# Kernel tuning notes

Hardware: AMD Instinct MI355X
Metric: run time of the kernel (lower is better)

The kernel has to match this reference:

```python
import jax, jax.numpy as jnp
import numpy as np

ALPHA = 0.2  # LeakyReLU negative slope
NEG_INF = -1e12


def setup_inputs() -> dict:
    key = jax.random.key(0)
    k1, k2, k3, k4, k5 = jax.random.split(key, 5)
    N, F = 4096, 512
    inp = jax.random.normal(k1, (N, F), dtype=jnp.float32)
    adj = jax.random.randint(k2, (N, N), 0, 2).astype(jnp.float32)
    W = jax.random.normal(k3, (F, F), dtype=jnp.float32) * (1.414 / np.sqrt(F))
    a = jax.random.normal(k4, (2 * F, 1), dtype=jnp.float32) * 0.05
    wtrans = jax.random.normal(k5, (2 * F, F), dtype=jnp.float32) * (1.414 / np.sqrt(1.5 * F))
    return {"inp": inp, "adj": adj, "W": W, "a": a, "wtrans": wtrans}


def reference(inp, adj, W, a, wtrans):
    F_out = W.shape[1]
    h = inp @ W                                   # [N, F]
    Wh1 = h @ a[:F_out, :]                        # [N, 1]
    Wh2 = h @ a[F_out:, :]                        # [N, 1]
    e = jax.nn.leaky_relu(Wh1 + Wh2.T, ALPHA)     # [N, N]
    mask = adj > 0
    attention = jax.nn.softmax(jnp.where(mask, e, NEG_INF), axis=1)
    negative_attention = -jax.nn.softmax(jnp.where(mask, -e, NEG_INF), axis=1)
    # dropout p=0.0 (eval mode): identity
    h_prime = attention @ inp                     # [N, F_in]
    h_prime_negative = negative_attention @ inp   # [N, F_in]
    h_prime_double = jnp.concatenate([h_prime, h_prime_negative], axis=1)
    new_h_prime = h_prime_double @ wtrans         # [N, F_out]
    return jax.nn.elu(new_h_prime)
```

## Files before the change

kernel.cpp:

```cpp
#include <hip/hip_runtime.h>
#include <hip/hip_bf16.h>

#define N_NODES 4096
#define F_DIM   512
#define KTOT    8192
#define KSPLIT  8
#define LOG2E   1.44269504f

typedef __attribute__((ext_vector_type(8))) short bf16x8;
typedef __attribute__((ext_vector_type(4))) float f32x4;

__device__ inline unsigned short f2bf(float f) {
  union { float f; unsigned u; } c; c.f = f;
  unsigned r = c.u + 0x7fffu + ((c.u >> 16) & 1u);
  return (unsigned short)(r >> 16);
}
__device__ inline float bf2f(unsigned short u) {
  union { unsigned u; float f; } c; c.u = ((unsigned)u) << 16;
  return c.f;
}

__global__ void k_compute_v(const float* __restrict__ W, const float* __restrict__ a,
                            float* __restrict__ v1, float* __restrict__ v2) {
  int r = blockIdx.x, l = threadIdx.x;
  float s1 = 0.f, s2 = 0.f;
  for (int c = l; c < F_DIM; c += 64) {
    float w = W[(size_t)r * F_DIM + c];
    s1 += w * a[c];
    s2 += w * a[F_DIM + c];
  }
#pragma unroll
  for (int off = 32; off > 0; off >>= 1) { s1 += __shfl_down(s1, off); s2 += __shfl_down(s2, off); }
  if (l == 0) { v1[r] = s1; v2[r] = s2; }
}

__global__ void k_compute_wh(const float* __restrict__ inp, const float* __restrict__ v1,
                             const float* __restrict__ v2, float* __restrict__ Wh1,
                             float* __restrict__ Wh2) {
  int i = blockIdx.x, l = threadIdx.x;
  float s1 = 0.f, s2 = 0.f;
  for (int c = l; c < F_DIM; c += 64) {
    float x = inp[(size_t)i * F_DIM + c];
    s1 += x * v1[c];
    s2 += x * v2[c];
  }
#pragma unroll
  for (int off = 32; off > 0; off >>= 1) { s1 += __shfl_down(s1, off); s2 += __shfl_down(s2, off); }
  if (l == 0) { Wh1[i] = s1 * LOG2E; Wh2[i] = s2 * LOG2E; }
}

__global__ void k_transpose_bf16(const float* __restrict__ src, unsigned short* __restrict__ dst,
                                 int R, int C) {
  __shared__ float tile[32][33];
  int c0 = blockIdx.x * 32, r0 = blockIdx.y * 32;
  int tx = threadIdx.x, ty = threadIdx.y;
#pragma unroll
  for (int i = ty; i < 32; i += 8)
    tile[i][tx] = src[(size_t)(r0 + i) * C + c0 + tx];
  __syncthreads();
#pragma unroll
  for (int i = ty; i < 32; i += 8)
    dst[(size_t)(c0 + i) * R + r0 + tx] = f2bf(tile[tx][i]);
}

__global__ __launch_bounds__(256) void k_y(const float* __restrict__ inp,
                                           const unsigned short* __restrict__ wtT,
                                           unsigned short* __restrict__ YT) {
  int tid = threadIdx.x, l = tid & 63, w = tid >> 6;
  int row = l & 15, kg = l >> 4;
  int jt = blockIdx.x * 64 + w * 16;
  int cb = blockIdx.y * 64;
  f32x4 acc1[4] = {}, acc2[4] = {};
  const float* ap = inp + (size_t)(jt + row) * F_DIM + kg * 8;
  for (int k0 = 0; k0 < F_DIM; k0 += 32) {
    float4 f0 = *(const float4*)(ap + k0);
    float4 f1 = *(const float4*)(ap + k0 + 4);
    bf16x8 a;
    a[0] = (short)f2bf(f0.x); a[1] = (short)f2bf(f0.y); a[2] = (short)f2bf(f0.z); a[3] = (short)f2bf(f0.w);
    a[4] = (short)f2bf(f1.x); a[5] = (short)f2bf(f1.y); a[6] = (short)f2bf(f1.z); a[7] = (short)f2bf(f1.w);
#pragma unroll
    for (int n = 0; n < 4; n++) {
      const unsigned short* bp = wtT + (size_t)(cb + n * 16 + row) * 1024 + kg * 8 + k0;
      bf16x8 b1 = *(const bf16x8*)(bp);
      bf16x8 b2 = *(const bf16x8*)(bp + F_DIM);
      acc1[n] = __builtin_amdgcn_mfma_f32_16x16x32_bf16(a, b1, acc1[n], 0, 0, 0);
      acc2[n] = __builtin_amdgcn_mfma_f32_16x16x32_bf16(a, b2, acc2[n], 0, 0, 0);
    }
  }
  int jb = jt + kg * 4;
#pragma unroll
  for (int n = 0; n < 4; n++) {
    int f = cb + n * 16 + row;
    ushort4 o1, o2;
    o1.x = f2bf(acc1[n][0]); o1.y = f2bf(acc1[n][1]); o1.z = f2bf(acc1[n][2]); o1.w = f2bf(acc1[n][3]);
    o2.x = f2bf(acc2[n][0]); o2.y = f2bf(acc2[n][1]); o2.z = f2bf(acc2[n][2]); o2.w = f2bf(acc2[n][3]);
    *(ushort4*)(YT + (size_t)f * KTOT + jb) = o1;
    *(ushort4*)(YT + (size_t)f * KTOT + 4096 + jb) = o2;
  }
}

__global__ __launch_bounds__(256) void k_p(const float* __restrict__ adj,
                                           const float* __restrict__ Wh1,
                                           const float* __restrict__ Wh2,
                                           unsigned short* __restrict__ Pcat) {
  int i = blockIdx.x, t = threadIdx.x;
  float w1 = Wh1[i];
  int j0 = t * 16;
  const float* ar = adj + (size_t)i * N_NODES + j0;
  float4 A0 = *(const float4*)(ar);
  float4 A1 = *(const float4*)(ar + 4);
  float4 A2 = *(const float4*)(ar + 8);
  float4 A3 = *(const float4*)(ar + 12);
  float am[16] = {A0.x, A0.y, A0.z, A0.w, A1.x, A1.y, A1.z, A1.w,
                  A2.x, A2.y, A2.z, A2.w, A3.x, A3.y, A3.z, A3.w};
  float4 wv0 = *(const float4*)(Wh2 + j0);
  float4 wv1 = *(const float4*)(Wh2 + j0 + 4);
  float4 wv2 = *(const float4*)(Wh2 + j0 + 8);
  float4 wv3 = *(const float4*)(Wh2 + j0 + 12);
  float w2[16] = {wv0.x, wv0.y, wv0.z, wv0.w, wv1.x, wv1.y, wv1.z, wv1.w,
                  wv2.x, wv2.y, wv2.z, wv2.w, wv3.x, wv3.y, wv3.z, wv3.w};
  float pe[16], ne[16];
  float sp = 0.f, sn = 0.f;
#pragma unroll
  for (int r = 0; r < 16; r++) {
    float s = w1 + w2[r];
    float e = fmaxf(s, 0.2f * s);
    float p = exp2f(e);
    float n = exp2f(-e);
    if (!(am[r] > 0.f)) { p = 0.f; n = 0.f; }
    pe[r] = p; ne[r] = n; sp += p; sn += n;
  }
#pragma unroll
  for (int off = 1; off < 64; off <<= 1) { sp += __shfl_xor(sp, off); sn += __shfl_xor(sn, off); }
  __shared__ float red[2][4];
  int wv = t >> 6, ln = t & 63;
  if (ln == 0) { red[0][wv] = sp; red[1][wv] = sn; }
  __syncthreads();
  sp = red[0][0] + red[0][1] + red[0][2] + red[0][3];
  sn = red[1][0] + red[1][1] + red[1][2] + red[1][3];
  float rp = 1.f / sp;
  float rn = -1.f / sn;
  bf16x8 o;
#pragma unroll
  for (int r = 0; r < 8; r++) o[r] = (short)f2bf(pe[r] * rp);
  *(bf16x8*)(Pcat + (size_t)i * KTOT + j0) = o;
#pragma unroll
  for (int r = 0; r < 8; r++) o[r] = (short)f2bf(pe[8 + r] * rp);
  *(bf16x8*)(Pcat + (size_t)i * KTOT + j0 + 8) = o;
#pragma unroll
  for (int r = 0; r < 8; r++) o[r] = (short)f2bf(ne[r] * rn);
  *(bf16x8*)(Pcat + (size_t)i * KTOT + 4096 + j0) = o;
#pragma unroll
  for (int r = 0; r < 8; r++) o[r] = (short)f2bf(ne[8 + r] * rn);
  *(bf16x8*)(Pcat + (size_t)i * KTOT + 4096 + j0 + 8) = o;
}

#define GLOAD16(gp, lp) __builtin_amdgcn_global_load_lds( \
    (const __attribute__((address_space(1))) unsigned int*)(gp), \
    (__attribute__((address_space(3))) unsigned int*)(lp), 16, 0, 0)

__global__ __launch_bounds__(256) void k_pv(const unsigned short* __restrict__ Pcat,
                                            const unsigned short* __restrict__ YT,
                                            unsigned short* __restrict__ part) {
  __shared__ unsigned short Ab[2][128 * 32];
  __shared__ unsigned short Bb[2][128 * 32];
  const int kchunk = KTOT / KSPLIT;
  int t = threadIdx.x;
  int l = t & 63, w = t >> 6;
  int la = l & 15, kg = l >> 4;
  int wr = w >> 1, wc = w & 1;
  int bm0 = blockIdx.x * 128, bn0 = blockIdx.y * 128;
  size_t kbase = (size_t)blockIdx.z * kchunk;
  const int nsteps = kchunk / 32;

  int seg = ((t & 3) ^ ((t >> 3) & 3)) << 4;
  const char* gA = (const char*)Pcat + ((size_t)(bm0 + (t >> 2)) * KTOT + kbase) * 2 + seg;
  const char* gB = (const char*)YT   + ((size_t)(bn0 + (t >> 2)) * KTOT + kbase) * 2 + seg;
  const size_t rstep = (size_t)64 * KTOT * 2;

  int aswz = (kg ^ ((la >> 1) & 3)) << 4;
  int abase = (wr * 64 + la) * 64 + aswz;
  int bbase = (wc * 64 + la) * 64 + aswz;

  f32x4 acc[4][4] = {};

#define STAGE(buf, st) do { \
    const char* _ga = gA + (size_t)(st) * 64; \
    const char* _gb = gB + (size_t)(st) * 64; \
    char* _la = (char*)&Ab[buf][0] + w * 1024; \
    char* _lb = (char*)&Bb[buf][0] + w * 1024; \
    GLOAD16(_ga, _la); \
    GLOAD16(_ga + rstep, _la + 4096); \
    GLOAD16(_gb, _lb); \
    GLOAD16(_gb + rstep, _lb + 4096); \
  } while (0)

  STAGE(0, 0);
  __syncthreads();
  for (int st = 0; st < nsteps; st++) {
    int cur = st & 1;
    if (st + 1 < nsteps) STAGE(cur ^ 1, st + 1);
    const char* Abp = (const char*)&Ab[cur][0];
    const char* Bbp = (const char*)&Bb[cur][0];
    bf16x8 af[4], bfr[4];
#pragma unroll
    for (int mi = 0; mi < 4; mi++) af[mi] = *(const bf16x8*)(Abp + abase + mi * 16 * 64);
#pragma unroll
    for (int ni = 0; ni < 4; ni++) bfr[ni] = *(const bf16x8*)(Bbp + bbase + ni * 16 * 64);
#pragma unroll
    for (int mi = 0; mi < 4; mi++)
#pragma unroll
      for (int ni = 0; ni < 4; ni++)
        acc[mi][ni] = __builtin_amdgcn_mfma_f32_16x16x32_bf16(af[mi], bfr[ni], acc[mi][ni], 0, 0, 0);
    __syncthreads();
  }

  unsigned short* po = part + (size_t)blockIdx.z * (N_NODES * F_DIM);
#pragma unroll
  for (int mi = 0; mi < 4; mi++)
#pragma unroll
    for (int ni = 0; ni < 4; ni++)
#pragma unroll
      for (int r = 0; r < 4; r++) {
        int i_ = bm0 + wr * 64 + mi * 16 + kg * 4 + r;
        int f_ = bn0 + wc * 64 + ni * 16 + la;
        po[(size_t)i_ * F_DIM + f_] = f2bf(acc[mi][ni][r]);
      }
}

__global__ __launch_bounds__(256) void k_fin(const unsigned short* __restrict__ part,
                                             float* __restrict__ out) {
  size_t idx = ((size_t)blockIdx.x * 256 + threadIdx.x) * 8;
  float s[8] = {};
#pragma unroll
  for (int p = 0; p < KSPLIT; p++) {
    bf16x8 v = *(const bf16x8*)(part + (size_t)p * (N_NODES * F_DIM) + idx);
#pragma unroll
    for (int r = 0; r < 8; r++) s[r] += bf2f((unsigned short)v[r]);
  }
#pragma unroll
  for (int r = 0; r < 8; r++) s[r] = s[r] > 0.f ? s[r] : (__expf(s[r]) - 1.f);
  float4 o0 = make_float4(s[0], s[1], s[2], s[3]);
  float4 o1 = make_float4(s[4], s[5], s[6], s[7]);
  *(float4*)(out + idx) = o0;
  *(float4*)(out + idx + 4) = o1;
}

extern "C" void kernel_launch(void* const* d_in, const int* in_sizes, int n_in,
                              void* d_out, int out_size, void* d_ws, size_t ws_size,
                              hipStream_t stream) {
  (void)in_sizes; (void)n_in; (void)out_size; (void)ws_size;
  const float* inp    = (const float*)d_in[0];
  const float* adj    = (const float*)d_in[1];
  const float* W      = (const float*)d_in[2];
  const float* a      = (const float*)d_in[3];
  const float* wtrans = (const float*)d_in[4];
  float* out = (float*)d_out;

  char* ws = (char*)d_ws;
  float* v1  = (float*)ws;
  float* v2  = (float*)(ws + 2048);
  float* Wh1 = (float*)(ws + 4096);
  float* Wh2 = (float*)(ws + 20480);

  const size_t PSZ = (size_t)N_NODES * F_DIM * 2;
  char* regA = ws + 65536;
  unsigned short* wtT  = (unsigned short*)regA;
  unsigned short* part = (unsigned short*)regA;
  unsigned short* YT   = (unsigned short*)(regA + KSPLIT * PSZ);
  unsigned short* Pcat = (unsigned short*)(regA + KSPLIT * PSZ + 8388608);

  k_compute_v<<<512, 64, 0, stream>>>(W, a, v1, v2);
  k_compute_wh<<<4096, 64, 0, stream>>>(inp, v1, v2, Wh1, Wh2);
  k_transpose_bf16<<<dim3(16, 32), dim3(32, 8), 0, stream>>>(wtrans, wtT, 1024, F_DIM);
  k_y<<<dim3(64, 8), 256, 0, stream>>>(inp, wtT, YT);
  k_p<<<4096, 256, 0, stream>>>(adj, Wh1, Wh2, Pcat);
  k_pv<<<dim3(32, 4, KSPLIT), 256, 0, stream>>>(Pcat, YT, part);
  k_fin<<<1024, 256, 0, stream>>>(part, out);
}
```

Measured before the change: 136.4 us.

## Enlarge PV GEMM tiles to 256x256 with triple-buffered async LDS pipeline

Doubles the split-K PV GEMM block tile to 256x256 with 512 threads (8 waves, each computing 128x64). LDS staging moves from double to triple buffering, with explicit vmcnt waits and raw barriers in place of a full syncthreads. MFMA sections are raised in priority with s_setprio. The goal is more data reuse per loaded byte and better overlap of global-to-LDS loads with MFMA work. In exchange the grid shrinks to 256 blocks, and register and LDS use per block grow.

```diff
diff --git a/kernel.cpp b/kernel.cpp
--- a/kernel.cpp
+++ b/kernel.cpp
@@ -159,70 +159,81 @@
     (const __attribute__((address_space(1))) unsigned int*)(gp), \
     (__attribute__((address_space(3))) unsigned int*)(lp), 16, 0, 0)
 
-__global__ __launch_bounds__(256) void k_pv(const unsigned short* __restrict__ Pcat,
-                                            const unsigned short* __restrict__ YT,
-                                            unsigned short* __restrict__ part) {
-  __shared__ unsigned short Ab[2][128 * 32];
-  __shared__ unsigned short Bb[2][128 * 32];
+__global__ __launch_bounds__(512, 2) void k_pv(const unsigned short* __restrict__ Pcat,
+                                               const unsigned short* __restrict__ YT,
+                                               unsigned short* __restrict__ part) {
+  __shared__ unsigned short Ab[3][256 * 32];
+  __shared__ unsigned short Bb[3][256 * 32];
   const int kchunk = KTOT / KSPLIT;
   int t = threadIdx.x;
   int l = t & 63, w = t >> 6;
   int la = l & 15, kg = l >> 4;
-  int wr = w >> 1, wc = w & 1;
-  int bm0 = blockIdx.x * 128, bn0 = blockIdx.y * 128;
+  int wr = w >> 2, wc = w & 3;
+  int bm0 = blockIdx.x * 256, bn0 = blockIdx.y * 256;
   size_t kbase = (size_t)blockIdx.z * kchunk;
   const int nsteps = kchunk / 32;
 
   int seg = ((t & 3) ^ ((t >> 3) & 3)) << 4;
   const char* gA = (const char*)Pcat + ((size_t)(bm0 + (t >> 2)) * KTOT + kbase) * 2 + seg;
   const char* gB = (const char*)YT   + ((size_t)(bn0 + (t >> 2)) * KTOT + kbase) * 2 + seg;
-  const size_t rstep = (size_t)64 * KTOT * 2;
+  const size_t rstep = (size_t)128 * KTOT * 2;
 
   int aswz = (kg ^ ((la >> 1) & 3)) << 4;
-  int abase = (wr * 64 + la) * 64 + aswz;
+  int abase = (wr * 128 + la) * 64 + aswz;
   int bbase = (wc * 64 + la) * 64 + aswz;
 
-  f32x4 acc[4][4] = {};
-
-#define STAGE(buf, st) do { \
+  f32x4 acc[8][4] = {};
+
+#define STAGE3(buf, st) do { \
     const char* _ga = gA + (size_t)(st) * 64; \
     const char* _gb = gB + (size_t)(st) * 64; \
     char* _la = (char*)&Ab[buf][0] + w * 1024; \
     char* _lb = (char*)&Bb[buf][0] + w * 1024; \
     GLOAD16(_ga, _la); \
-    GLOAD16(_ga + rstep, _la + 4096); \
+    GLOAD16(_ga + rstep, _la + 8192); \
     GLOAD16(_gb, _lb); \
-    GLOAD16(_gb + rstep, _lb + 4096); \
+    GLOAD16(_gb + rstep, _lb + 8192); \
   } while (0)
 
-  STAGE(0, 0);
-  __syncthreads();
+  STAGE3(0, 0);
+  STAGE3(1, 1);
   for (int st = 0; st < nsteps; st++) {
-    int cur = st & 1;
-    if (st + 1 < nsteps) STAGE(cur ^ 1, st + 1);
-    const char* Abp = (const char*)&Ab[cur][0];
-    const char* Bbp = (const char*)&Bb[cur][0];
-    bf16x8 af[4], bfr[4];
-#pragma unroll
-    for (int mi = 0; mi < 4; mi++) af[mi] = *(const bf16x8*)(Abp + abase + mi * 16 * 64);
-#pragma unroll
-    for (int ni = 0; ni < 4; ni++) bfr[ni] = *(const bf16x8*)(Bbp + bbase + ni * 16 * 64);
-#pragma unroll
-    for (int mi = 0; mi < 4; mi++)
+    __builtin_amdgcn_s_barrier();
+    int buf = st % 3;
+    if (st + 2 < nsteps) {
+      STAGE3((st + 2) % 3, st + 2);
+      asm volatile("s_waitcnt vmcnt(8)" ::: "memory");
+    } else if (st + 1 < nsteps) {
+      asm volatile("s_waitcnt vmcnt(4)" ::: "memory");
+    } else {
+      asm volatile("s_waitcnt vmcnt(0)" ::: "memory");
+    }
+    __builtin_amdgcn_s_barrier();
+
+    const char* Abp = (const char*)&Ab[buf][0];
+    const char* Bbp = (const char*)&Bb[buf][0];
+    bf16x8 af[8], bfr[4];
+#pragma unroll
+    for (int mi = 0; mi < 8; mi++) af[mi] = *(const bf16x8*)(Abp + abase + mi * 1024);
+#pragma unroll
+    for (int ni = 0; ni < 4; ni++) bfr[ni] = *(const bf16x8*)(Bbp + bbase + ni * 1024);
+    __builtin_amdgcn_s_setprio(1);
+#pragma unroll
+    for (int mi = 0; mi < 8; mi++)
 #pragma unroll
       for (int ni = 0; ni < 4; ni++)
         acc[mi][ni] = __builtin_amdgcn_mfma_f32_16x16x32_bf16(af[mi], bfr[ni], acc[mi][ni], 0, 0, 0);
-    __syncthreads();
+    __builtin_amdgcn_s_setprio(0);
   }
 
   unsigned short* po = part + (size_t)blockIdx.z * (N_NODES * F_DIM);
 #pragma unroll
-  for (int mi = 0; mi < 4; mi++)
+  for (int mi = 0; mi < 8; mi++)
 #pragma unroll
     for (int ni = 0; ni < 4; ni++)
 #pragma unroll
       for (int r = 0; r < 4; r++) {
-        int i_ = bm0 + wr * 64 + mi * 16 + kg * 4 + r;
+        int i_ = bm0 + wr * 128 + mi * 16 + kg * 4 + r;
         int f_ = bn0 + wc * 64 + ni * 16 + la;
         po[(size_t)i_ * F_DIM + f_] = f2bf(acc[mi][ni][r]);
       }
@@ -275,6 +286,6 @@
   k_transpose_bf16<<<dim3(16, 32), dim3(32, 8), 0, stream>>>(wtrans, wtT, 1024, F_DIM);
   k_y<<<dim3(64, 8), 256, 0, stream>>>(inp, wtT, YT);
   k_p<<<4096, 256, 0, stream>>>(adj, Wh1, Wh2, Pcat);
-  k_pv<<<dim3(32, 4, KSPLIT), 256, 0, stream>>>(Pcat, YT, part);
+  k_pv<<<dim3(16, 2, KSPLIT), 512, 0, stream>>>(Pcat, YT, part);
   k_fin<<<1024, 256, 0, stream>>>(part, out);
 }
```

After: 130.1 us. -4.6%, faster.
